# Kernel optimization log

Measured on AMD Instinct MI355X. Metric: run time of the kernel, lower is better.

## Reference

```python
import jax, jax.numpy as jnp
import numpy as np

N = 8192
IN_F = 512
NFEAT = 512
OUT_F = 512


def setup_inputs() -> dict:
    key = jax.random.key(0)
    k1, k2, k3, k4, k5 = jax.random.split(key, 5)
    stdv = 1.0 / np.sqrt(OUT_F)
    return {
        "input": jax.random.normal(k1, (N, IN_F), dtype=jnp.float32),
        "adj": jax.random.uniform(k2, (N, N), dtype=jnp.float32),
        "x": jax.random.normal(k3, (N, NFEAT), dtype=jnp.float32),
        "weight": jax.random.uniform(k4, (IN_F + N + NFEAT, OUT_F), minval=-stdv, maxval=stdv, dtype=jnp.float32),
        "bias": jax.random.uniform(k5, (OUT_F,), minval=-stdv, maxval=stdv, dtype=jnp.float32),
    }


def reference(input, adj, x, weight, bias):
    # support = [adj @ input | adj | x]  -> [n, in_features + n + nfeat]
    support = jnp.concatenate((adj @ input, adj, x), axis=1)
    return support @ weight + bias
```

## Files before the change

kernel.cpp:

```cpp
#include <hip/hip_runtime.h>
#include <hip/hip_bf16.h>

typedef __attribute__((ext_vector_type(4))) float f32x4;
typedef __attribute__((ext_vector_type(8))) short bf16x8;
typedef __attribute__((ext_vector_type(4))) unsigned short u16x4;
typedef __attribute__((ext_vector_type(8))) unsigned short u16x8;

__device__ __forceinline__ unsigned short f2bf(float f) {
    unsigned int u = __builtin_bit_cast(unsigned int, f);
    u += 0x7fffu + ((u >> 16) & 1u);
    return (unsigned short)(u >> 16);
}

#define SWZ(i) ((i) ^ ((((i) >> 6) & 7) << 3))

__global__ void transpose_cvt(const float* __restrict__ src,
                              unsigned short* __restrict__ dst,
                              int rows, int cols, int ltw) {
    int idx = blockIdx.x * 256 + threadIdx.x;
    int n = idx / rows;
    int k = idx - n * rows;
    unsigned short v = f2bf(src[(size_t)k * cols + n]);
    int tw = 1 << ltw;
    int tile = (n >> ltw) * (rows >> 6) + (k >> 6);
    dst[(size_t)tile * (tw * 64) + SWZ((n & (tw - 1)) * 64 + (k & 63))] = v;
}

template<int EPI>
__global__ __launch_bounds__(512, 4)
void gemm_small(const float* __restrict__ A, long lda,
                const unsigned short* __restrict__ Bt,
                int K,
                const float* __restrict__ epi, long lde,
                const float* __restrict__ bias,
                void* __restrict__ Dptr, long ldd) {
    __shared__ unsigned short sA[2][64 * 64];
    __shared__ unsigned short sB[2][128 * 64];

    const int t = threadIdx.x;
    const int l = t & 63;
    const int w = t >> 6;
    const int wm = w >> 2;
    const int wn = w & 3;

    int mt, nt;
    {
        int lin = blockIdx.y * gridDim.x + blockIdx.x;
        int xcd = lin & 7;
        int slot = lin >> 3;
        int ppx = gridDim.y >> 3;
        mt = xcd * ppx + slot / gridDim.x;
        nt = slot % gridDim.x;
    }
    const long m0 = (long)mt * 64;
    const long n0 = (long)nt * 128;
    const int KT = K >> 6;
    const unsigned short* Bblk = Bt + (size_t)nt * KT * 8192;

    f32x4 acc[2][2];
    #pragma unroll
    for (int m = 0; m < 2; ++m)
        #pragma unroll
        for (int n = 0; n < 2; ++n)
            acc[m][n] = {0.f, 0.f, 0.f, 0.f};

    f32x4 aX0, aX1, aY0, aY1;

    auto gll_B = [&](int kt, int buf) {
        const unsigned short* src = Bblk + (size_t)kt * 8192 + t * 8;
        #pragma unroll
        for (int r = 0; r < 2; ++r)
            __builtin_amdgcn_global_load_lds(
                (const __attribute__((address_space(1))) void*)(src + r * 4096),
                (__attribute__((address_space(3))) void*)&sB[buf][r * 4096 + w * 512],
                16, 0, 0);
    };

    auto load_A = [&](int kt, f32x4& a0, f32x4& a1) {
        const float* p0 = &A[(m0 + (t >> 4)) * lda + (long)kt * 64 + ((t & 15) << 2)];
        const float* p1 = p0 + 32 * lda;
        asm volatile("global_load_dwordx4 %0, %2, off\n\t"
                     "global_load_dwordx4 %1, %3, off"
                     : "=&v"(a0), "=&v"(a1)
                     : "v"(p0), "v"(p1)
                     : "memory");
    };

    auto write_A = [&](int buf, const f32x4& a0, const f32x4& a1) {
        int e0 = t * 4;
        u16x4 w0 = {f2bf(a0[0]), f2bf(a0[1]), f2bf(a0[2]), f2bf(a0[3])};
        *reinterpret_cast<u16x4*>(&sA[buf][SWZ(e0)]) = w0;
        int e1 = 2048 + t * 4;
        u16x4 w1 = {f2bf(a1[0]), f2bf(a1[1]), f2bf(a1[2]), f2bf(a1[3])};
        *reinterpret_cast<u16x4*>(&sA[buf][SWZ(e1)]) = w1;
    };

    auto compute = [&](int buf) {
        #pragma unroll
        for (int kk = 0; kk < 2; ++kk) {
            bf16x8 af[2], bfr[2];
            const int kb = kk * 32 + ((l >> 4) << 3);
            #pragma unroll
            for (int m = 0; m < 2; ++m) {
                int row = wm * 32 + m * 16 + (l & 15);
                af[m] = *reinterpret_cast<const bf16x8*>(&sA[buf][SWZ(row * 64 + kb)]);
            }
            #pragma unroll
            for (int n = 0; n < 2; ++n) {
                int col = wn * 32 + n * 16 + (l & 15);
                bfr[n] = *reinterpret_cast<const bf16x8*>(&sB[buf][SWZ(col * 64 + kb)]);
            }
            __builtin_amdgcn_s_setprio(1);
            #pragma unroll
            for (int m = 0; m < 2; ++m)
                #pragma unroll
                for (int n = 0; n < 2; ++n)
                    acc[m][n] = __builtin_amdgcn_mfma_f32_16x16x32_bf16(
                        af[m], bfr[n], acc[m][n], 0, 0, 0);
            __builtin_amdgcn_s_setprio(0);
        }
    };

    gll_B(0, 0);
    load_A(0, aX0, aX1);
    load_A(1, aY0, aY1);
    asm volatile("s_waitcnt vmcnt(2)" ::: "memory");
    __builtin_amdgcn_sched_barrier(0);
    write_A(0, aX0, aX1);
    asm volatile("s_waitcnt lgkmcnt(0)" ::: "memory");
    __builtin_amdgcn_s_barrier();
    __builtin_amdgcn_sched_barrier(0);

    const int nk = K >> 6;
    for (int p = 0; p + 2 < nk; p += 2) {
        gll_B(p + 1, 1);
        load_A(p + 2, aX0, aX1);
        compute(0);
        asm volatile("s_waitcnt vmcnt(4)" ::: "memory");
        __builtin_amdgcn_sched_barrier(0);
        write_A(1, aY0, aY1);
        asm volatile("s_waitcnt vmcnt(2) lgkmcnt(0)" ::: "memory");
        __builtin_amdgcn_s_barrier();
        __builtin_amdgcn_sched_barrier(0);

        gll_B(p + 2, 0);
        load_A(p + 3, aY0, aY1);
        compute(1);
        asm volatile("s_waitcnt vmcnt(4)" ::: "memory");
        __builtin_amdgcn_sched_barrier(0);
        write_A(0, aX0, aX1);
        asm volatile("s_waitcnt vmcnt(2) lgkmcnt(0)" ::: "memory");
        __builtin_amdgcn_s_barrier();
        __builtin_amdgcn_sched_barrier(0);
    }

    gll_B(nk - 1, 1);
    compute(0);
    asm volatile("s_waitcnt vmcnt(2)" ::: "memory");
    __builtin_amdgcn_sched_barrier(0);
    write_A(1, aY0, aY1);
    asm volatile("s_waitcnt vmcnt(0) lgkmcnt(0)" ::: "memory");
    __builtin_amdgcn_s_barrier();
    __builtin_amdgcn_sched_barrier(0);
    compute(1);

    const int jrow = (l >> 4) * 4;
    #pragma unroll
    for (int m = 0; m < 2; ++m) {
        const long row = m0 + wm * 32 + m * 16 + jrow;
        #pragma unroll
        for (int n = 0; n < 2; ++n) {
            const long col = n0 + wn * 32 + n * 16 + (l & 15);
            f32x4 v = acc[m][n];
            if constexpr (EPI == 0) {
                u16x4 o;
                #pragma unroll
                for (int j = 0; j < 4; ++j)
                    o[j] = f2bf(v[j] + epi[(row + j) * lde + col]);
                int tile = ((int)col >> 8) * 128 + ((int)row >> 6);
                int idx = ((int)col & 255) * 64 + ((int)row & 63);
                *reinterpret_cast<u16x4*>(
                    &((unsigned short*)Dptr)[(size_t)tile * 16384 + SWZ(idx)]) = o;
            } else {
                float b = bias[col];
                #pragma unroll
                for (int j = 0; j < 4; ++j)
                    ((float*)Dptr)[(row + j) * ldd + col] = v[j] + b;
            }
        }
    }
}

__global__ __launch_bounds__(512, 2)
void gemm_big(const float* __restrict__ A,
              const unsigned short* __restrict__ Bt,
              float* __restrict__ Out) {
    __shared__ unsigned short sA[2][256 * 64];
    __shared__ unsigned short sB[2][256 * 64];

    const int t = threadIdx.x;
    const int l = t & 63;
    const int w = t >> 6;
    const int wm = w & 3;
    const int wn = w >> 2;

    const int lin = blockIdx.x;
    const int slot = lin & 7;
    const int kq = slot & 3;
    const int mhalf = slot >> 1 >> 1;
    const int idx = lin >> 3;
    const int nt = idx & 1;
    const int mt = mhalf * 16 + (idx >> 1);

    const long m0 = (long)mt * 256;
    const long k0 = (long)kq * 2048;
    const int n0 = nt * 256;
    const int ktbase = nt * 128 + kq * 32;
    constexpr int P = 32;

    f32x4 acc[4][8];
    #pragma unroll
    for (int mi = 0; mi < 4; ++mi)
        #pragma unroll
        for (int ni = 0; ni < 8; ++ni)
            acc[mi][ni] = {0.f, 0.f, 0.f, 0.f};

    f32x4 avH[8];

    auto gll_B = [&](int ph, int buf) {
        const unsigned short* src = Bt + ((size_t)(ktbase + ph)) * 16384 + t * 8;
        #pragma unroll
        for (int r = 0; r < 4; ++r)
            __builtin_amdgcn_global_load_lds(
                (const __attribute__((address_space(1))) void*)(src + r * 4096),
                (__attribute__((address_space(3))) void*)&sB[buf][r * 4096 + w * 512],
                16, 0, 0);
    };

    auto load_A = [&](int ph) {
        const float* base = A + m0 * 8192 + k0 + (long)ph * 64;
        #pragma unroll
        for (int j = 0; j < 8; ++j) {
            int chunk = j * 512 + t;
            int row = chunk >> 4;
            int kc = (chunk & 15) << 2;
            const float* p = base + (long)row * 8192 + kc;
            asm volatile("global_load_dwordx4 %0, %1, off"
                         : "=&v"(avH[j]) : "v"(p) : "memory");
        }
    };

    auto write_A = [&](int buf) {
        #pragma unroll
        for (int j = 0; j < 8; ++j) {
            int chunk = j * 512 + t;
            int row = chunk >> 4;
            int kc = (chunk & 15) << 2;
            int idx2 = row * 64 + kc;
            u16x4 wv = {f2bf(avH[j][0]), f2bf(avH[j][1]), f2bf(avH[j][2]), f2bf(avH[j][3])};
            *reinterpret_cast<u16x4*>(&sA[buf][SWZ(idx2)]) = wv;
        }
    };

    auto compute = [&](int buf) {
        #pragma unroll
        for (int kk = 0; kk < 2; ++kk) {
            const int kb = kk * 32 + ((l >> 4) << 3);
            bf16x8 af[4], bf[8];
            #pragma unroll
            for (int mi = 0; mi < 4; ++mi) {
                int row = wm * 64 + mi * 16 + (l & 15);
                af[mi] = *reinterpret_cast<const bf16x8*>(&sA[buf][SWZ(row * 64 + kb)]);
            }
            #pragma unroll
            for (int ni = 0; ni < 8; ++ni) {
                int col = wn * 128 + ni * 16 + (l & 15);
                bf[ni] = *reinterpret_cast<const bf16x8*>(&sB[buf][SWZ(col * 64 + kb)]);
            }
            __builtin_amdgcn_s_setprio(1);
            #pragma unroll
            for (int mi = 0; mi < 4; ++mi)
                #pragma unroll
                for (int ni = 0; ni < 8; ++ni)
                    acc[mi][ni] = __builtin_amdgcn_mfma_f32_16x16x32_bf16(
                        af[mi], bf[ni], acc[mi][ni], 0, 0, 0);
            __builtin_amdgcn_s_setprio(0);
        }
    };

    load_A(0);
    gll_B(0, 0);
    asm volatile("s_waitcnt vmcnt(4)" ::: "memory");
    __builtin_amdgcn_sched_barrier(0);
    write_A(0);
    load_A(1);
    asm volatile("s_waitcnt vmcnt(8) lgkmcnt(0)" ::: "memory");
    __builtin_amdgcn_s_barrier();
    __builtin_amdgcn_sched_barrier(0);

    for (int p = 0; p < P - 2; ++p) {
        gll_B(p + 1, (p + 1) & 1);
        asm volatile("s_waitcnt vmcnt(4)" ::: "memory");
        __builtin_amdgcn_sched_barrier(0);
        write_A((p + 1) & 1);
        load_A(p + 2);
        compute(p & 1);
        asm volatile("s_waitcnt vmcnt(8) lgkmcnt(0)" ::: "memory");
        __builtin_amdgcn_s_barrier();
        __builtin_amdgcn_sched_barrier(0);
    }

    gll_B(P - 1, (P - 1) & 1);
    asm volatile("s_waitcnt vmcnt(4)" ::: "memory");
    __builtin_amdgcn_sched_barrier(0);
    write_A((P - 1) & 1);
    compute((P - 2) & 1);
    asm volatile("s_waitcnt vmcnt(0) lgkmcnt(0)" ::: "memory");
    __builtin_amdgcn_s_barrier();
    __builtin_amdgcn_sched_barrier(0);

    compute((P - 1) & 1);

    #pragma unroll
    for (int mi = 0; mi < 4; ++mi) {
        const long row0 = m0 + wm * 64 + mi * 16 + ((l >> 4) << 2);
        #pragma unroll
        for (int ni = 0; ni < 8; ++ni) {
            const int col = n0 + wn * 128 + ni * 16 + (l & 15);
            #pragma unroll
            for (int j = 0; j < 4; ++j)
                unsafeAtomicAdd(&Out[(row0 + j) * 512 + col], acc[mi][ni][j]);
        }
    }
}

extern "C" void kernel_launch(void* const* d_in, const int* in_sizes, int n_in,
                              void* d_out, int out_size, void* d_ws, size_t ws_size,
                              hipStream_t stream) {
    const float* input  = (const float*)d_in[0];
    const float* adj    = (const float*)d_in[1];
    const float* x      = (const float*)d_in[2];
    const float* weight = (const float*)d_in[3];
    const float* bias   = (const float*)d_in[4];

    const int N = 8192, IN_F = 512, NFEAT = 512, OUT_F = 512;
    float* out = (float*)d_out;

    unsigned short* Tbt = (unsigned short*)d_ws;
    unsigned short* W1t = Tbt + (size_t)2 * 128 * 16384;
    unsigned short* W3t = W1t + (size_t)4 * 8 * 8192;

    transpose_cvt<<<dim3((IN_F * OUT_F) / 256), dim3(256), 0, stream>>>(
        weight, W1t, IN_F, OUT_F, 7);
    transpose_cvt<<<dim3((NFEAT * OUT_F) / 256), dim3(256), 0, stream>>>(
        weight + (size_t)(IN_F + N) * OUT_F, W3t, NFEAT, OUT_F, 7);

    dim3 grid(OUT_F / 128, N / 64);

    gemm_small<1><<<grid, 512, 0, stream>>>(
        x, (long)NFEAT, W3t, NFEAT,
        nullptr, 0, bias,
        out, (long)OUT_F);

    gemm_small<0><<<grid, 512, 0, stream>>>(
        input, (long)IN_F, W1t, IN_F,
        weight + (size_t)IN_F * OUT_F, (long)OUT_F, nullptr,
        Tbt, 0);

    gemm_big<<<dim3(256), dim3(512), 0, stream>>>(adj, Tbt, out);
}
```

Measured before the change: 182.9 us.

## Pre-pack adj to bf16 tiles in chunks and stream both operands via LDS DMA

Adds a pack_adj kernel that converts adj column-chunks to swizzled bf16 tiles in workspace. The big GEMM then loads both A and B with global_load_lds, with no register staging or in-kernel conversion. Tiles shrink to 128x256, and the work is split into 2 or 4 sequential pack+GEMM launches depending on workspace size. This aims to simplify the main loop and improve overlap. The cost is an extra full read of adj plus a bf16 write and re-read, more launches, and smaller tiles with fewer blocks per launch.

```diff
diff --git a/kernel.cpp b/kernel.cpp
--- a/kernel.cpp
+++ b/kernel.cpp
@@ -24,6 +24,26 @@
     int tw = 1 << ltw;
     int tile = (n >> ltw) * (rows >> 6) + (k >> 6);
     dst[(size_t)tile * (tw * 64) + SWZ((n & (tw - 1)) * 64 + (k & 63))] = v;
+}
+
+__global__ __launch_bounds__(256)
+void pack_adj(const float* __restrict__ src, unsigned short* __restrict__ dst,
+              int chunk_off, int iters, int KQC) {
+    const int t = threadIdx.x;
+    const int b = blockIdx.x;
+    #pragma unroll
+    for (int r4 = 0; r4 < 4; ++r4) {
+        const int row = b * 4 + r4;
+        const int mt = row >> 7, r = row & 127;
+        const float* srow = src + (size_t)row * 8192 + chunk_off;
+        for (int it = 0; it < iters; ++it) {
+            f32x4 v = *reinterpret_cast<const f32x4*>(&srow[it * 1024 + t * 4]);
+            u16x4 o = {f2bf(v[0]), f2bf(v[1]), f2bf(v[2]), f2bf(v[3])};
+            int tile = (mt * KQC + (it >> 1)) * 32 + (it & 1) * 16 + (t >> 4);
+            *reinterpret_cast<u16x4*>(&dst[(size_t)tile * 8192 +
+                                           SWZ(r * 64 + (t & 15) * 4)]) = o;
+        }
+    }
 }
 
 template<int EPI>
@@ -191,142 +211,103 @@
     }
 }
 
-__global__ __launch_bounds__(512, 2)
-void gemm_big(const float* __restrict__ A,
+__global__ __launch_bounds__(512, 1)
+void gemm_big(const unsigned short* __restrict__ Abt,
               const unsigned short* __restrict__ Bt,
-              float* __restrict__ Out) {
-    __shared__ unsigned short sA[2][256 * 64];
+              float* __restrict__ Out,
+              int cbase, int KQC) {
+    __shared__ unsigned short sA[2][128 * 64];
     __shared__ unsigned short sB[2][256 * 64];
 
     const int t = threadIdx.x;
     const int l = t & 63;
     const int w = t >> 6;
-    const int wm = w & 3;
-    const int wn = w >> 2;
+    const int wm = w & 1;
+    const int wn = w >> 1;
 
     const int lin = blockIdx.x;
     const int slot = lin & 7;
-    const int kq = slot & 3;
-    const int mhalf = slot >> 1 >> 1;
     const int idx = lin >> 3;
+    const int kql = slot & (KQC - 1);
+    const int mpart = slot >> (KQC - 1);
     const int nt = idx & 1;
-    const int mt = mhalf * 16 + (idx >> 1);
-
-    const long m0 = (long)mt * 256;
-    const long k0 = (long)kq * 2048;
-    const int n0 = nt * 256;
-    const int ktbase = nt * 128 + kq * 32;
-    constexpr int P = 32;
-
-    f32x4 acc[4][8];
+    const int mt = mpart * 8 * KQC + (idx >> 1);
+
+    const unsigned short* Ab = Abt + (size_t)(mt * KQC + kql) * 32 * 8192;
+    const int ktb = nt * 128 + cbase + kql * 32;
+
+    f32x4 acc[4][4];
     #pragma unroll
     for (int mi = 0; mi < 4; ++mi)
         #pragma unroll
-        for (int ni = 0; ni < 8; ++ni)
+        for (int ni = 0; ni < 4; ++ni)
             acc[mi][ni] = {0.f, 0.f, 0.f, 0.f};
 
-    f32x4 avH[8];
-
-    auto gll_B = [&](int ph, int buf) {
-        const unsigned short* src = Bt + ((size_t)(ktbase + ph)) * 16384 + t * 8;
+    auto gll_AB = [&](int p, int buf) {
+        const unsigned short* sa = Ab + (size_t)p * 8192 + t * 8;
+        #pragma unroll
+        for (int r = 0; r < 2; ++r)
+            __builtin_amdgcn_global_load_lds(
+                (const __attribute__((address_space(1))) void*)(sa + r * 4096),
+                (__attribute__((address_space(3))) void*)&sA[buf][r * 4096 + w * 512],
+                16, 0, 0);
+        const unsigned short* sb = Bt + (size_t)(ktb + p) * 16384 + t * 8;
         #pragma unroll
         for (int r = 0; r < 4; ++r)
             __builtin_amdgcn_global_load_lds(
-                (const __attribute__((address_space(1))) void*)(src + r * 4096),
+                (const __attribute__((address_space(1))) void*)(sb + r * 4096),
                 (__attribute__((address_space(3))) void*)&sB[buf][r * 4096 + w * 512],
                 16, 0, 0);
     };
 
-    auto load_A = [&](int ph) {
-        const float* base = A + m0 * 8192 + k0 + (long)ph * 64;
-        #pragma unroll
-        for (int j = 0; j < 8; ++j) {
-            int chunk = j * 512 + t;
-            int row = chunk >> 4;
-            int kc = (chunk & 15) << 2;
-            const float* p = base + (long)row * 8192 + kc;
-            asm volatile("global_load_dwordx4 %0, %1, off"
-                         : "=&v"(avH[j]) : "v"(p) : "memory");
-        }
-    };
-
-    auto write_A = [&](int buf) {
-        #pragma unroll
-        for (int j = 0; j < 8; ++j) {
-            int chunk = j * 512 + t;
-            int row = chunk >> 4;
-            int kc = (chunk & 15) << 2;
-            int idx2 = row * 64 + kc;
-            u16x4 wv = {f2bf(avH[j][0]), f2bf(avH[j][1]), f2bf(avH[j][2]), f2bf(avH[j][3])};
-            *reinterpret_cast<u16x4*>(&sA[buf][SWZ(idx2)]) = wv;
-        }
-    };
-
     auto compute = [&](int buf) {
         #pragma unroll
         for (int kk = 0; kk < 2; ++kk) {
             const int kb = kk * 32 + ((l >> 4) << 3);
-            bf16x8 af[4], bf[8];
+            bf16x8 af[4], bf[4];
             #pragma unroll
             for (int mi = 0; mi < 4; ++mi) {
                 int row = wm * 64 + mi * 16 + (l & 15);
                 af[mi] = *reinterpret_cast<const bf16x8*>(&sA[buf][SWZ(row * 64 + kb)]);
             }
             #pragma unroll
-            for (int ni = 0; ni < 8; ++ni) {
-                int col = wn * 128 + ni * 16 + (l & 15);
+            for (int ni = 0; ni < 4; ++ni) {
+                int col = wn * 64 + ni * 16 + (l & 15);
                 bf[ni] = *reinterpret_cast<const bf16x8*>(&sB[buf][SWZ(col * 64 + kb)]);
             }
             __builtin_amdgcn_s_setprio(1);
             #pragma unroll
             for (int mi = 0; mi < 4; ++mi)
                 #pragma unroll
-                for (int ni = 0; ni < 8; ++ni)
+                for (int ni = 0; ni < 4; ++ni)
                     acc[mi][ni] = __builtin_amdgcn_mfma_f32_16x16x32_bf16(
                         af[mi], bf[ni], acc[mi][ni], 0, 0, 0);
             __builtin_amdgcn_s_setprio(0);
         }
     };
 
-    load_A(0);
-    gll_B(0, 0);
-    asm volatile("s_waitcnt vmcnt(4)" ::: "memory");
-    __builtin_amdgcn_sched_barrier(0);
-    write_A(0);
-    load_A(1);
-    asm volatile("s_waitcnt vmcnt(8) lgkmcnt(0)" ::: "memory");
+    gll_AB(0, 0);
+    for (int p = 0; p < 31; ++p) {
+        gll_AB(p + 1, (p + 1) & 1);
+        asm volatile("s_waitcnt vmcnt(6)" ::: "memory");
+        __builtin_amdgcn_sched_barrier(0);
+        __builtin_amdgcn_s_barrier();
+        __builtin_amdgcn_sched_barrier(0);
+        compute(p & 1);
+        __builtin_amdgcn_s_barrier();
+    }
+    asm volatile("s_waitcnt vmcnt(0)" ::: "memory");
+    __builtin_amdgcn_sched_barrier(0);
     __builtin_amdgcn_s_barrier();
     __builtin_amdgcn_sched_barrier(0);
-
-    for (int p = 0; p < P - 2; ++p) {
-        gll_B(p + 1, (p + 1) & 1);
-        asm volatile("s_waitcnt vmcnt(4)" ::: "memory");
-        __builtin_amdgcn_sched_barrier(0);
-        write_A((p + 1) & 1);
-        load_A(p + 2);
-        compute(p & 1);
-        asm volatile("s_waitcnt vmcnt(8) lgkmcnt(0)" ::: "memory");
-        __builtin_amdgcn_s_barrier();
-        __builtin_amdgcn_sched_barrier(0);
-    }
-
-    gll_B(P - 1, (P - 1) & 1);
-    asm volatile("s_waitcnt vmcnt(4)" ::: "memory");
-    __builtin_amdgcn_sched_barrier(0);
-    write_A((P - 1) & 1);
-    compute((P - 2) & 1);
-    asm volatile("s_waitcnt vmcnt(0) lgkmcnt(0)" ::: "memory");
-    __builtin_amdgcn_s_barrier();
-    __builtin_amdgcn_sched_barrier(0);
-
-    compute((P - 1) & 1);
+    compute(1);
 
     #pragma unroll
     for (int mi = 0; mi < 4; ++mi) {
-        const long row0 = m0 + wm * 64 + mi * 16 + ((l >> 4) << 2);
-        #pragma unroll
-        for (int ni = 0; ni < 8; ++ni) {
-            const int col = n0 + wn * 128 + ni * 16 + (l & 15);
+        const long row0 = (long)mt * 128 + wm * 64 + mi * 16 + ((l >> 4) << 2);
+        #pragma unroll
+        for (int ni = 0; ni < 4; ++ni) {
+            const int col = nt * 256 + wn * 64 + ni * 16 + (l & 15);
             #pragma unroll
             for (int j = 0; j < 4; ++j)
                 unsafeAtomicAdd(&Out[(row0 + j) * 512 + col], acc[mi][ni][j]);
@@ -346,9 +327,16 @@
     const int N = 8192, IN_F = 512, NFEAT = 512, OUT_F = 512;
     float* out = (float*)d_out;
 
-    unsigned short* Tbt = (unsigned short*)d_ws;
-    unsigned short* W1t = Tbt + (size_t)2 * 128 * 16384;
-    unsigned short* W3t = W1t + (size_t)4 * 8 * 8192;
+    const size_t fixedBytes = (size_t)512 * 8192 * 2 + 2 * (size_t)512 * 512 * 2;
+    int NC = (ws_size >= (size_t)8192 * 4096 * 2 + fixedBytes) ? 2 : 4;
+    const int KQC = (NC == 2) ? 2 : 1;
+    const int chunkK = 8192 / NC;
+    const size_t chunkBytes = (size_t)8192 * chunkK * 2;
+
+    unsigned short* Abt = (unsigned short*)d_ws;
+    unsigned short* Tbt = (unsigned short*)((char*)d_ws + chunkBytes);
+    unsigned short* W1t = Tbt + (size_t)OUT_F * N;
+    unsigned short* W3t = W1t + (size_t)OUT_F * IN_F;
 
     transpose_cvt<<<dim3((IN_F * OUT_F) / 256), dim3(256), 0, stream>>>(
         weight, W1t, IN_F, OUT_F, 7);
@@ -367,5 +355,11 @@
         weight + (size_t)IN_F * OUT_F, (long)OUT_F, nullptr,
         Tbt, 0);
 
-    gemm_big<<<dim3(256), dim3(512), 0, stream>>>(adj, Tbt, out);
-}
+    const int nBlocks = 64 * 2 * KQC;
+    for (int c = 0; c < NC; ++c) {
+        pack_adj<<<dim3(2048), dim3(256), 0, stream>>>(
+            adj, Abt, c * chunkK, chunkK / 1024, KQC);
+        gemm_big<<<dim3(nBlocks), dim3(512), 0, stream>>>(
+            Abt, Tbt, out, c * (128 / NC), KQC);
+    }
+}
```

Measured after the change: 255.0 us. +39.4%, slower.

## Shrink big GEMM tile to 128x256, single-buffer A, raise occupancy

Applied to the files above, without the earlier changes.

The large adj GEMM now uses 128-row M tiles with a 2x4 wave layout and 4x4 MFMA accumulators per wave, and launches twice as many blocks with launch bounds raised to allow 4 blocks per CU. The A tile in LDS becomes single-buffered. The loop is reordered so compute happens first, followed by a barrier, then the A write and the next A/B loads, which puts B prefetch two stages ahead. Block-to-tile mapping groups M tiles per XCD. The aim is more occupancy and better latency hiding, paid for with lower per-block reuse: adj is now read twice per N-half with smaller tiles, and there is an extra barrier per iteration.

```diff
diff --git a/kernel.cpp b/kernel.cpp
--- a/kernel.cpp
+++ b/kernel.cpp
@@ -16,14 +16,13 @@
 
 __global__ void transpose_cvt(const float* __restrict__ src,
                               unsigned short* __restrict__ dst,
-                              int rows, int cols, int ltw) {
+                              int rows, int cols) {
     int idx = blockIdx.x * 256 + threadIdx.x;
     int n = idx / rows;
     int k = idx - n * rows;
     unsigned short v = f2bf(src[(size_t)k * cols + n]);
-    int tw = 1 << ltw;
-    int tile = (n >> ltw) * (rows >> 6) + (k >> 6);
-    dst[(size_t)tile * (tw * 64) + SWZ((n & (tw - 1)) * 64 + (k & 63))] = v;
+    int tile = (n >> 7) * (rows >> 6) + (k >> 6);
+    dst[(size_t)tile * 8192 + SWZ((n & 127) * 64 + (k & 63))] = v;
 }
 
 template<int EPI>
@@ -191,44 +190,43 @@
     }
 }
 
-__global__ __launch_bounds__(512, 2)
+__global__ __launch_bounds__(512, 4)
 void gemm_big(const float* __restrict__ A,
               const unsigned short* __restrict__ Bt,
               float* __restrict__ Out) {
-    __shared__ unsigned short sA[2][256 * 64];
+    __shared__ unsigned short sA[128 * 64];
     __shared__ unsigned short sB[2][256 * 64];
 
     const int t = threadIdx.x;
     const int l = t & 63;
     const int w = t >> 6;
-    const int wm = w & 3;
-    const int wn = w >> 2;
+    const int wm = w & 1;
+    const int wn = w >> 1;
 
     const int lin = blockIdx.x;
-    const int slot = lin & 7;
-    const int kq = slot & 3;
-    const int mhalf = slot >> 1 >> 1;
+    const int xcd = lin & 7;
     const int idx = lin >> 3;
-    const int nt = idx & 1;
-    const int mt = mhalf * 16 + (idx >> 1);
-
-    const long m0 = (long)mt * 256;
+    const int mt = xcd * 8 + (idx & 7);
+    const int rest = idx >> 3;
+    const int nt = rest & 1;
+    const int kq = rest >> 1;
+
+    const long m0 = (long)mt * 128;
     const long k0 = (long)kq * 2048;
-    const int n0 = nt * 256;
-    const int ktbase = nt * 128 + kq * 32;
+    const unsigned short* Bblk = Bt + ((size_t)(nt * 128 + kq * 32)) * 16384;
     constexpr int P = 32;
 
-    f32x4 acc[4][8];
+    f32x4 acc[4][4];
     #pragma unroll
     for (int mi = 0; mi < 4; ++mi)
         #pragma unroll
-        for (int ni = 0; ni < 8; ++ni)
+        for (int ni = 0; ni < 4; ++ni)
             acc[mi][ni] = {0.f, 0.f, 0.f, 0.f};
 
-    f32x4 avH[8];
-
-    auto gll_B = [&](int ph, int buf) {
-        const unsigned short* src = Bt + ((size_t)(ktbase + ph)) * 16384 + t * 8;
+    f32x4 avH[4];
+
+    auto gll_B = [&](int p, int buf) {
+        const unsigned short* src = Bblk + (size_t)p * 16384 + t * 8;
         #pragma unroll
         for (int r = 0; r < 4; ++r)
             __builtin_amdgcn_global_load_lds(
@@ -237,28 +235,26 @@
                 16, 0, 0);
     };
 
-    auto load_A = [&](int ph) {
-        const float* base = A + m0 * 8192 + k0 + (long)ph * 64;
-        #pragma unroll
-        for (int j = 0; j < 8; ++j) {
+    auto load_A = [&](int p) {
+        #pragma unroll
+        for (int j = 0; j < 4; ++j) {
             int chunk = j * 512 + t;
             int row = chunk >> 4;
             int kc = (chunk & 15) << 2;
-            const float* p = base + (long)row * 8192 + kc;
+            const float* ptr = A + (m0 + row) * 8192 + k0 + (long)p * 64 + kc;
             asm volatile("global_load_dwordx4 %0, %1, off"
-                         : "=&v"(avH[j]) : "v"(p) : "memory");
-        }
-    };
-
-    auto write_A = [&](int buf) {
-        #pragma unroll
-        for (int j = 0; j < 8; ++j) {
+                         : "=&v"(avH[j]) : "v"(ptr) : "memory");
+        }
+    };
+
+    auto write_A = [&]() {
+        #pragma unroll
+        for (int j = 0; j < 4; ++j) {
             int chunk = j * 512 + t;
-            int row = chunk >> 4;
-            int kc = (chunk & 15) << 2;
-            int idx2 = row * 64 + kc;
-            u16x4 wv = {f2bf(avH[j][0]), f2bf(avH[j][1]), f2bf(avH[j][2]), f2bf(avH[j][3])};
-            *reinterpret_cast<u16x4*>(&sA[buf][SWZ(idx2)]) = wv;
+            int e = (chunk >> 4) * 64 + ((chunk & 15) << 2);
+            u16x4 wv = {f2bf(avH[j][0]), f2bf(avH[j][1]),
+                        f2bf(avH[j][2]), f2bf(avH[j][3])};
+            *reinterpret_cast<u16x4*>(&sA[SWZ(e)]) = wv;
         }
     };
 
@@ -266,24 +262,24 @@
         #pragma unroll
         for (int kk = 0; kk < 2; ++kk) {
             const int kb = kk * 32 + ((l >> 4) << 3);
-            bf16x8 af[4], bf[8];
+            bf16x8 af[4], bfr[4];
             #pragma unroll
             for (int mi = 0; mi < 4; ++mi) {
                 int row = wm * 64 + mi * 16 + (l & 15);
-                af[mi] = *reinterpret_cast<const bf16x8*>(&sA[buf][SWZ(row * 64 + kb)]);
-            }
-            #pragma unroll
-            for (int ni = 0; ni < 8; ++ni) {
-                int col = wn * 128 + ni * 16 + (l & 15);
-                bf[ni] = *reinterpret_cast<const bf16x8*>(&sB[buf][SWZ(col * 64 + kb)]);
+                af[mi] = *reinterpret_cast<const bf16x8*>(&sA[SWZ(row * 64 + kb)]);
+            }
+            #pragma unroll
+            for (int ni = 0; ni < 4; ++ni) {
+                int col = wn * 64 + ni * 16 + (l & 15);
+                bfr[ni] = *reinterpret_cast<const bf16x8*>(&sB[buf][SWZ(col * 64 + kb)]);
             }
             __builtin_amdgcn_s_setprio(1);
             #pragma unroll
             for (int mi = 0; mi < 4; ++mi)
                 #pragma unroll
-                for (int ni = 0; ni < 8; ++ni)
+                for (int ni = 0; ni < 4; ++ni)
                     acc[mi][ni] = __builtin_amdgcn_mfma_f32_16x16x32_bf16(
-                        af[mi], bf[ni], acc[mi][ni], 0, 0, 0);
+                        af[mi], bfr[ni], acc[mi][ni], 0, 0, 0);
             __builtin_amdgcn_s_setprio(0);
         }
     };
@@ -292,29 +288,31 @@
     gll_B(0, 0);
     asm volatile("s_waitcnt vmcnt(4)" ::: "memory");
     __builtin_amdgcn_sched_barrier(0);
-    write_A(0);
+    write_A();
     load_A(1);
+    gll_B(1, 1);
     asm volatile("s_waitcnt vmcnt(8) lgkmcnt(0)" ::: "memory");
     __builtin_amdgcn_s_barrier();
     __builtin_amdgcn_sched_barrier(0);
 
     for (int p = 0; p < P - 2; ++p) {
-        gll_B(p + 1, (p + 1) & 1);
+        compute(p & 1);
+        __builtin_amdgcn_s_barrier();
         asm volatile("s_waitcnt vmcnt(4)" ::: "memory");
         __builtin_amdgcn_sched_barrier(0);
-        write_A((p + 1) & 1);
+        write_A();
         load_A(p + 2);
-        compute(p & 1);
+        gll_B(p + 2, p & 1);
         asm volatile("s_waitcnt vmcnt(8) lgkmcnt(0)" ::: "memory");
         __builtin_amdgcn_s_barrier();
         __builtin_amdgcn_sched_barrier(0);
     }
 
-    gll_B(P - 1, (P - 1) & 1);
+    compute((P - 2) & 1);
+    __builtin_amdgcn_s_barrier();
     asm volatile("s_waitcnt vmcnt(4)" ::: "memory");
     __builtin_amdgcn_sched_barrier(0);
-    write_A((P - 1) & 1);
-    compute((P - 2) & 1);
+    write_A();
     asm volatile("s_waitcnt vmcnt(0) lgkmcnt(0)" ::: "memory");
     __builtin_amdgcn_s_barrier();
     __builtin_amdgcn_sched_barrier(0);
@@ -325,8 +323,8 @@
     for (int mi = 0; mi < 4; ++mi) {
         const long row0 = m0 + wm * 64 + mi * 16 + ((l >> 4) << 2);
         #pragma unroll
-        for (int ni = 0; ni < 8; ++ni) {
-            const int col = n0 + wn * 128 + ni * 16 + (l & 15);
+        for (int ni = 0; ni < 4; ++ni) {
+            const int col = nt * 256 + wn * 64 + ni * 16 + (l & 15);
             #pragma unroll
             for (int j = 0; j < 4; ++j)
                 unsafeAtomicAdd(&Out[(row0 + j) * 512 + col], acc[mi][ni][j]);
@@ -347,13 +345,13 @@
     float* out = (float*)d_out;
 
     unsigned short* Tbt = (unsigned short*)d_ws;
-    unsigned short* W1t = Tbt + (size_t)2 * 128 * 16384;
-    unsigned short* W3t = W1t + (size_t)4 * 8 * 8192;
+    unsigned short* W1t = Tbt + (size_t)OUT_F * N;
+    unsigned short* W3t = W1t + (size_t)OUT_F * IN_F;
 
     transpose_cvt<<<dim3((IN_F * OUT_F) / 256), dim3(256), 0, stream>>>(
-        weight, W1t, IN_F, OUT_F, 7);
+        weight, W1t, IN_F, OUT_F);
     transpose_cvt<<<dim3((NFEAT * OUT_F) / 256), dim3(256), 0, stream>>>(
-        weight + (size_t)(IN_F + N) * OUT_F, W3t, NFEAT, OUT_F, 7);
+        weight + (size_t)(IN_F + N) * OUT_F, W3t, NFEAT, OUT_F);
 
     dim3 grid(OUT_F / 128, N / 64);
 
@@ -367,5 +365,5 @@
         weight + (size_t)IN_F * OUT_F, (long)OUT_F, nullptr,
         Tbt, 0);
 
-    gemm_big<<<dim3(256), dim3(512), 0, stream>>>(adj, Tbt, out);
-}
+    gemm_big<<<dim3(512), dim3(512), 0, stream>>>(adj, Tbt, out);
+}
```

Measured after the change: 227.5 us. 24.4% more time.
